# Kernel tuning notes

Hardware: AMD Instinct MI355X
Metric: run time of the kernel (lower is better)

The kernel has to match this reference:

```python
import jax, jax.numpy as jnp
import numpy as np

D_MODEL = 256
N_HEADS = 8
D_K = 16
LN_EPS = 1e-5


def setup_inputs() -> dict:
    key = jax.random.key(0)
    ks = jax.random.split(key, 10)
    B, S = 4, 2048
    inp = {
        "input_Q": jax.random.normal(ks[0], (B, S, D_MODEL), dtype=jnp.float32),
        "input_K": jax.random.normal(ks[1], (B, S, D_MODEL), dtype=jnp.float32),
        "input_V": jax.random.normal(ks[2], (B, S, D_MODEL), dtype=jnp.float32),
        "attn_mask": jax.random.randint(ks[3], (B, S, S), 0, 2) == 1,
        # learned params (torch Linear weight [out,in] stored here as [in,out])
        "Wq": jax.random.normal(ks[4], (D_MODEL, N_HEADS * D_K), dtype=jnp.float32) * (1.0 / np.sqrt(D_MODEL)),
        "Wk": jax.random.normal(ks[5], (D_MODEL, N_HEADS * D_K), dtype=jnp.float32) * (1.0 / np.sqrt(D_MODEL)),
        "Wv": jax.random.normal(ks[6], (D_MODEL, N_HEADS * D_K), dtype=jnp.float32) * (1.0 / np.sqrt(D_MODEL)),
        "Wfc": jax.random.normal(ks[7], (N_HEADS * D_K, D_MODEL), dtype=jnp.float32) * (1.0 / np.sqrt(N_HEADS * D_K)),
        "ln_gamma": jnp.ones((D_MODEL,), dtype=jnp.float32),
        "ln_beta": jnp.zeros((D_MODEL,), dtype=jnp.float32),
    }
    return inp


def reference(input_Q, input_K, input_V, attn_mask, Wq, Wk, Wv, Wfc, ln_gamma, ln_beta):
    B, S, _ = input_Q.shape
    # projections -> [B, H, S, d_k]
    Q = (input_Q @ Wq).reshape(B, S, N_HEADS, D_K).transpose(0, 2, 1, 3)
    K = (input_K @ Wk).reshape(B, S, N_HEADS, D_K).transpose(0, 2, 1, 3)
    V = (input_V @ Wv).reshape(B, S, N_HEADS, D_K).transpose(0, 2, 1, 3)
    # scores [B, H, S, S], masked softmax
    scores = jnp.einsum("bhqd,bhkd->bhqk", Q, K) / np.sqrt(D_K).astype(np.float32)
    scores = jnp.where(attn_mask[:, None, :, :], jnp.float32(-1e9), scores)
    attn = jax.nn.softmax(scores, axis=-1)
    context = jnp.einsum("bhqk,bhkd->bhqd", attn, V)
    context = context.transpose(0, 2, 1, 3).reshape(B, S, N_HEADS * D_K)
    out = context @ Wfc
    # LayerNorm (no residual in the original module)
    mu = jnp.mean(out, axis=-1, keepdims=True)
    var = jnp.var(out, axis=-1, keepdims=True)
    out = (out - mu) * jax.lax.rsqrt(var + LN_EPS) * ln_gamma + ln_beta
    return out
```

## Files before the change

### kernel.cpp

```cpp
#include <hip/hip_runtime.h>
#include <hip/hip_bf16.h>

#define S_LEN 2048
#define BATCH 4
#define NH 8
#define DK 16
#define DM 256
#define DP 128
#define L2E 1.4426950408889634f

typedef short bf16x8 __attribute__((ext_vector_type(8)));
typedef short short4v __attribute__((ext_vector_type(4)));
typedef float f32x16 __attribute__((ext_vector_type(16)));

__device__ __forceinline__ short f2bf(float x) {
    __hip_bfloat16 h = __float2bfloat16(x);
    return __builtin_bit_cast(short, h);
}

union Frag { bf16x8 v; short4v h2[2]; };

__global__ __launch_bounds__(256) void prep(
    const void* __restrict__ mraw, unsigned long long* __restrict__ ms64,
    const float* __restrict__ Wq, const float* __restrict__ Wk,
    const float* __restrict__ Wv, short* __restrict__ Wt,
    short* __restrict__ Vb)
{
    __shared__ int isBool;
    const int bi = blockIdx.x;
    const int t = threadIdx.x;

    if (bi < 512) {
        const int tid = bi * 256 + t;
        const int bh = tid >> 12;
        const int rem = tid & 4095;
        const int row = 16 + (rem >> 11) * 4;
        const int s = rem & 2047;
        Vb[((size_t)bh * 32 + row) * S_LEN + s] = (short)0x3F80;
    } else if (bi < 560) {
        const int tid = (bi - 512) * 256 + t;
        const int c  = tid & 127;
        const int hi = (tid >> 7) & 1;
        const int kb = (tid >> 8) & 15;
        const int m  = tid >> 12;
        const float* W = (m == 0) ? Wq : (m == 1) ? Wk : Wv;
        const float scale = (m == 0) ? 0.25f * L2E : 1.0f;
        const int k0 = kb * 16 + 4 * hi;
        union { bf16x8 v; short s[8]; } o;
        #pragma unroll
        for (int e = 0; e < 4; ++e) {
            o.s[e]     = f2bf(W[(size_t)(k0 + e) * DP + c] * scale);
            o.s[4 + e] = f2bf(W[(size_t)(k0 + 8 + e) * DP + c] * scale);
        }
        *(bf16x8*)(Wt + (size_t)tid * 8) = o.v;
    } else {
        const size_t kbase0 = (size_t)(bi - 560) * 4096;
        if (t == 0) isBool = 0;
        __syncthreads();
        {
            unsigned int u = ((const unsigned int*)mraw)[(kbase0 >> 2) + t * 4];
            if (u & 0xFFFFFF00u) isBool = 1;
        }
        __syncthreads();

        const int lane = t & 63;
        const size_t kbase = kbase0 + (size_t)(t >> 6) * 1024;
        int v[16];
        if (!isBool) {
            const int* p = (const int*)mraw + kbase + lane;
            #pragma unroll
            for (int g = 0; g < 16; ++g) v[g] = p[g * 64];
        } else {
            const unsigned char* p = (const unsigned char*)mraw + kbase + lane;
            #pragma unroll
            for (int g = 0; g < 16; ++g) v[g] = p[g * 64];
        }

        const size_t row = kbase >> 11;
        const int w0 = (int)(kbase & 2047) >> 6;

        unsigned long long myw = 0;
        #pragma unroll
        for (int g = 0; g < 16; ++g) {
            const unsigned long long W = __ballot(v[g] != 0);
            myw = (lane == g) ? W : myw;
        }
        if (lane < 16) ms64[row * 32 + w0 + lane] = myw;
    }
}

__global__ __launch_bounds__(256) void proj_mfma(
    const float* __restrict__ Xq, const float* __restrict__ Xk, const float* __restrict__ Xv,
    const short* __restrict__ Wt,
    short* __restrict__ Qt, short* __restrict__ Kb, short* __restrict__ Vb)
{
    __shared__ short xs_s[32 * 260];
    const int bi = blockIdx.x;
    const int t = threadIdx.x;
    const int inp = bi >> 8;
    const int s0 = (bi & 255) * 32;

    {
        const float* xbase = ((inp == 0) ? Xq : (inp == 1) ? Xk : Xv) + (size_t)s0 * 256;
        #pragma unroll
        for (int u = 0; u < 8; ++u) {
            const int idx = u * 1024 + t * 4;
            const int row = idx >> 8, col = idx & 255;
            float4 xv = *(const float4*)(xbase + idx);
            short4v o = { f2bf(xv.x), f2bf(xv.y), f2bf(xv.z), f2bf(xv.w) };
            *(short4v*)&xs_s[row * 260 + col] = o;
        }
    }

    const int wave = t >> 6, lane = t & 63;
    const int lq = lane & 31, hi = lane >> 5;
    const int c = wave * 32 + lq;

    const short* w2 = Wt + (((size_t)inp * 16 * 2 + hi) * 128 + c) * 8;
    Frag wf[16];
    #pragma unroll
    for (int kb = 0; kb < 16; ++kb)
        wf[kb].v = *(const bf16x8*)(w2 + (size_t)kb * 2048);
    asm volatile("" ::: "memory");
    __syncthreads();

    f32x16 acc;
    #pragma unroll
    for (int i = 0; i < 16; ++i) acc[i] = 0.f;

    #pragma unroll
    for (int kb = 0; kb < 16; ++kb) {
        Frag af;
        af.h2[0] = *(const short4v*)&xs_s[lq * 260 + kb*16 + 4*hi];
        af.h2[1] = *(const short4v*)&xs_s[lq * 260 + kb*16 + 8 + 4*hi];
        acc = __builtin_amdgcn_mfma_f32_32x32x16_bf16(af.v, wf[kb].v, acc, 0, 0, 0);
    }

    const int b = s0 >> 11, sl = s0 & (S_LEN - 1);
    const int h = c >> 4, d = c & 15;
    if (inp == 1) {
        #pragma unroll
        for (int r = 0; r < 16; ++r) {
            const int s = sl + (r & 3) + 8*(r >> 2) + 4*hi;
            Kb[(((size_t)(b * NH + h)) * S_LEN + s) * DK + d] = f2bf(acc[r]);
        }
    } else {
        short* base = (inp == 0)
            ? Qt + (((size_t)(b * NH + h)) * 16 + d) * S_LEN + sl
            : Vb + (((size_t)(b * NH + h)) * 32 + d) * S_LEN + sl;
        #pragma unroll
        for (int g = 0; g < 4; ++g) {
            short4v vv = { f2bf(acc[4*g]), f2bf(acc[4*g+1]), f2bf(acc[4*g+2]), f2bf(acc[4*g+3]) };
            *(short4v*)(base + 8*g + 4*hi) = vv;
        }
    }
}

__global__ __launch_bounds__(256, 8) void attn_mfma(
    const short* __restrict__ Qt, const short* __restrict__ Kb, const short* __restrict__ Vb,
    const unsigned long long* __restrict__ ms64, float* __restrict__ pacc, float* __restrict__ pl)
{
    __shared__ short kt_s[128 * 20];
    __shared__ short vt_s[32 * 132];

    const int bh = blockIdx.y;
    const int b = bh >> 3;
    const int z = blockIdx.z;
    const int t = threadIdx.x;
    const int wave = t >> 6, lane = t & 63;
    const int lq = lane & 31, hi = lane >> 5;
    const int qrow = blockIdx.x * 128 + wave * 32 + lq;

    Frag qf;
    {
        const short* qt = Qt + (size_t)bh * 16 * S_LEN + qrow;
        #pragma unroll
        for (int j = 0; j < 4; ++j) {
            qf.h2[0][j] = qt[(size_t)(4*hi + j) * S_LEN];
            qf.h2[1][j] = qt[(size_t)(8 + 4*hi + j) * S_LEN];
        }
    }

    f32x16 acc;
    #pragma unroll
    for (int i = 0; i < 16; ++i) acc[i] = 0.f;

    const short* kbase = Kb + (size_t)bh * S_LEN * DK;
    const short* vbase = Vb + (size_t)bh * 32 * S_LEN;
    const unsigned long long* mrow = ms64 + ((size_t)b * S_LEN + qrow) * 32;

    const int tiles = (S_LEN / 128) / gridDim.z;
    const int t0 = z * tiles, t1 = t0 + tiles;

    for (int tile = t0; tile < t1; ++tile) {
        const int k0 = tile * 128;

        {
            const uint4 kv = *(const uint4*)(kbase + (size_t)k0 * DK + t * 8);
            short* kdst = &kt_s[(t >> 1) * 20 + (t & 1) * 8];
            *(uint2*)(kdst)     = *(uint2*)&kv;
            *(uint2*)(kdst + 4) = *((uint2*)&kv + 1);

            const short* vsrc = vbase + (size_t)(t >> 3) * S_LEN + k0 + (t & 7) * 16;
            uint4 v0 = *(const uint4*)(vsrc);
            uint4 v1 = *(const uint4*)(vsrc + 8);
            short* vdst = &vt_s[(t >> 3) * 132 + (t & 7) * 16];
            *(uint2*)(vdst)      = *(uint2*)&v0;
            *(uint2*)(vdst + 4)  = *((uint2*)&v0 + 1);
            *(uint2*)(vdst + 8)  = *(uint2*)&v1;
            *(uint2*)(vdst + 12) = *((uint2*)&v1 + 1);
        }
        __syncthreads();

        const ulonglong2 mw = *(const ulonglong2*)(mrow + tile * 2);
        const unsigned long long W64a = mw.x, W64b = mw.y;

        #pragma unroll
        for (int kt = 0; kt < 4; ++kt) {
            const unsigned int W = (unsigned int)(((kt < 2) ? W64a : W64b)
                                                  >> (32*(kt & 1) + 4*hi));
            f32x16 ci;
            #pragma unroll
            for (int r = 0; r < 16; ++r) {
                const int bit = (r & 3) + 8*(r >> 2);
                ci[r] = __int_as_float(((int)(W << (31 - bit)) >> 31) & 0xC2C80000);
            }

            Frag kf;
            kf.h2[0] = *(const short4v*)&kt_s[(kt*32 + lq) * 20 + 4*hi];
            kf.h2[1] = *(const short4v*)&kt_s[(kt*32 + lq) * 20 + 8 + 4*hi];
            f32x16 p = __builtin_amdgcn_mfma_f32_32x32x16_bf16(kf.v, qf.v, ci, 0, 0, 0);

            #pragma unroll
            for (int r = 0; r < 16; ++r) p[r] = __builtin_amdgcn_exp2f(p[r]);

            #pragma unroll
            for (int j = 0; j < 2; ++j) {
                union { bf16x8 v; unsigned int u[4]; } pf;
                #pragma unroll
                for (int e = 0; e < 4; ++e) {
                    asm("v_cvt_pk_bf16_f32 %0, %1, %2"
                        : "=v"(pf.u[e]) : "v"(p[j*8 + 2*e]), "v"(p[j*8 + 2*e + 1]));
                }
                Frag vf;
                const int vo = lq * 132 + (kt*2 + j) * 16 + 4*hi;
                vf.h2[0] = *(const short4v*)&vt_s[vo];
                vf.h2[1] = *(const short4v*)&vt_s[vo + 8];
                acc = __builtin_amdgcn_mfma_f32_32x32x16_bf16(vf.v, pf.v, acc, 0, 0, 0);
            }
        }
        __syncthreads();
    }

    float* pb = pacc + (((size_t)z * (BATCH*NH) + bh) * S_LEN + qrow) * 16;
    float4 o1 = { acc[0], acc[1], acc[2], acc[3] };
    float4 o2 = { acc[4], acc[5], acc[6], acc[7] };
    *(float4*)(pb + 4*hi) = o1;
    *(float4*)(pb + 8 + 4*hi) = o2;
    if (hi == 0) pl[((size_t)z * (BATCH*NH) + bh) * S_LEN + qrow] = acc[8];
}

__global__ __launch_bounds__(256) void fc_ln(
    const float* __restrict__ pacc, const float* __restrict__ pl, int ns,
    const float* __restrict__ Wfc,
    const float* __restrict__ gamma, const float* __restrict__ beta,
    float* __restrict__ out)
{
    __shared__ float cs[8][DP];
    __shared__ float ys[8][256];
    __shared__ float red[16];
    const int t = threadIdx.x;
    const int row0 = blockIdx.x * 8;

    {
        const int idx = t * 4;
        const int r = idx >> 7, k = idx & 127;
        const int grow = row0 + r;
        const int b = grow >> 11, q = grow & (S_LEN - 1);
        const int h = k >> 4, d0 = k & 15;
        float4 s = {0.f, 0.f, 0.f, 0.f};
        float L = 0.f;
        for (int z = 0; z < ns; ++z) {
            const size_t o = ((size_t)z * (BATCH*NH) + b * NH + h) * S_LEN + q;
            const float4 a = *(const float4*)(pacc + o * 16 + d0);
            s.x += a.x; s.y += a.y; s.z += a.z; s.w += a.w;
            L += pl[o];
        }
        const float inv = 1.0f / L;
        float4 o4 = { s.x * inv, s.y * inv, s.z * inv, s.w * inv };
        *(float4*)&cs[r][k] = o4;
    }
    __syncthreads();

    float acc[8] = {0,0,0,0,0,0,0,0};
    for (int k = 0; k < DP; k += 4) {
        const float w0 = Wfc[(k+0)*DM + t];
        const float w1 = Wfc[(k+1)*DM + t];
        const float w2 = Wfc[(k+2)*DM + t];
        const float w3 = Wfc[(k+3)*DM + t];
        #pragma unroll
        for (int r = 0; r < 8; ++r) {
            float4 x = *(const float4*)&cs[r][k];
            acc[r] = fmaf(x.x, w0, fmaf(x.y, w1, fmaf(x.z, w2, fmaf(x.w, w3, acc[r]))));
        }
    }

    #pragma unroll
    for (int r = 0; r < 8; ++r) ys[r][t] = acc[r];
    __syncthreads();

    const int w = t >> 6, lj = t & 63;
    #pragma unroll
    for (int rr = 0; rr < 2; ++rr) {
        const int r = w * 2 + rr;
        float a0 = ys[r][lj], a1 = ys[r][lj+64], a2 = ys[r][lj+128], a3 = ys[r][lj+192];
        float s1 = a0 + a1 + a2 + a3;
        float s2 = a0*a0 + a1*a1 + a2*a2 + a3*a3;
        #pragma unroll
        for (int off = 32; off; off >>= 1) {
            s1 += __shfl_xor(s1, off);
            s2 += __shfl_xor(s2, off);
        }
        if (lj == 0) {
            float mu = s1 * (1.0f/256.0f);
            float var = s2 * (1.0f/256.0f) - mu*mu;
            red[r*2]     = mu;
            red[r*2 + 1] = rsqrtf(var + 1e-5f);
        }
    }
    __syncthreads();

    const float g = gamma[t], be = beta[t];
    #pragma unroll
    for (int r = 0; r < 8; ++r) {
        float y = (acc[r] - red[r*2]) * red[r*2 + 1];
        out[(size_t)(row0 + r) * DM + t] = fmaf(y, g, be);
    }
}

extern "C" void kernel_launch(void* const* d_in, const int* in_sizes, int n_in,
                              void* d_out, int out_size, void* d_ws, size_t ws_size,
                              hipStream_t stream)
{
    const float* Xq = (const float*)d_in[0];
    const float* Xk = (const float*)d_in[1];
    const float* Xv = (const float*)d_in[2];
    const void* mask_raw = d_in[3];
    const float* Wq  = (const float*)d_in[4];
    const float* Wk  = (const float*)d_in[5];
    const float* Wv  = (const float*)d_in[6];
    const float* Wfc = (const float*)d_in[7];
    const float* gamma = (const float*)d_in[8];
    const float* beta  = (const float*)d_in[9];
    float* out = (float*)d_out;

    const size_t headsz = (size_t)BATCH * NH * S_LEN * DK;
    const size_t maskelems = (size_t)BATCH * S_LEN * S_LEN;

    char* wsb = (char*)d_ws;
    short* Qt = (short*)wsb;
    short* Kb = Qt + headsz;
    short* Vb = Kb + headsz;
    unsigned long long* msk = (unsigned long long*)(Vb + 2 * headsz);
    short* Wt = (short*)(msk + maskelems / 64);
    float* pacc = (float*)(Wt + 3 * 128 * 256);
    size_t ns = 4;
    {
        const size_t fixed = (size_t)((char*)pacc - wsb);
        while (ns > 1 && fixed + ns * ((size_t)BATCH*NH*S_LEN*17*4) > ws_size)
            ns >>= 1;
    }
    float* pl = pacc + ns * (size_t)BATCH * NH * S_LEN * 16;

    prep<<<dim3(512 + 48 + (unsigned)(maskelems / 4096)), dim3(256), 0, stream>>>(
        mask_raw, msk, Wq, Wk, Wv, Wt, Vb);
    proj_mfma<<<dim3(768), dim3(256), 0, stream>>>(Xq, Xk, Xv, Wt, Qt, Kb, Vb);
    attn_mfma<<<dim3(S_LEN / 128, BATCH * NH, (unsigned)ns), dim3(256), 0, stream>>>(
        Qt, Kb, Vb, msk, pacc, pl);
    fc_ln<<<dim3(BATCH * S_LEN / 8), dim3(256), 0, stream>>>(pacc, pl, (int)ns, Wfc, gamma, beta, out);
}
```

Measured before the change: 72.85 us.

## Use MFMA for output projection and merge mask packing into projection kernel

Replaces the scalar fp32 FC+LayerNorm kernel with a bf16 MFMA version that handles 32 rows per block and does the LayerNorm reduction through shuffles and shared memory. Wfc is pre-converted to bf16 fragments in the prep kernel. Mask bit-packing moves out of prep and into the projection kernel's grid, so the mask packing and the Q/K/V projection run concurrently in one launch. This trades fp32 precision in the FC matmul for bf16 and changes the store pattern for the output.

```diff
diff --git a/kernel.cpp b/kernel.cpp
--- a/kernel.cpp
+++ b/kernel.cpp
@@ -21,12 +21,10 @@
 union Frag { bf16x8 v; short4v h2[2]; };
 
 __global__ __launch_bounds__(256) void prep(
-    const void* __restrict__ mraw, unsigned long long* __restrict__ ms64,
     const float* __restrict__ Wq, const float* __restrict__ Wk,
-    const float* __restrict__ Wv, short* __restrict__ Wt,
-    short* __restrict__ Vb)
+    const float* __restrict__ Wv, const float* __restrict__ Wfc,
+    short* __restrict__ Wt, short* __restrict__ Wfcb, short* __restrict__ Vb)
 {
-    __shared__ int isBool;
     const int bi = blockIdx.x;
     const int t = threadIdx.x;
 
@@ -54,7 +52,91 @@
         }
         *(bf16x8*)(Wt + (size_t)tid * 8) = o.v;
     } else {
-        const size_t kbase0 = (size_t)(bi - 560) * 4096;
+        const int tid = (bi - 560) * 256 + t;
+        const int c  = tid & 255;
+        const int hi = (tid >> 8) & 1;
+        const int kb = tid >> 9;
+        const int k0 = kb * 16 + 4 * hi;
+        union { bf16x8 v; short s[8]; } o;
+        #pragma unroll
+        for (int e = 0; e < 4; ++e) {
+            o.s[e]     = f2bf(Wfc[(size_t)(k0 + e) * DM + c]);
+            o.s[4 + e] = f2bf(Wfc[(size_t)(k0 + 8 + e) * DM + c]);
+        }
+        *(bf16x8*)(Wfcb + (size_t)tid * 8) = o.v;
+    }
+}
+
+__global__ __launch_bounds__(256) void main1(
+    const void* __restrict__ mraw, unsigned long long* __restrict__ ms64,
+    const float* __restrict__ Xq, const float* __restrict__ Xk, const float* __restrict__ Xv,
+    const short* __restrict__ Wt,
+    short* __restrict__ Qt, short* __restrict__ Kb, short* __restrict__ Vb)
+{
+    __shared__ short xs_s[32 * 260];
+    __shared__ int isBool;
+    const int bi = blockIdx.x;
+    const int t = threadIdx.x;
+
+    if (bi < 768) {
+        const int inp = bi >> 8;
+        const int s0 = (bi & 255) * 32;
+        {
+            const float* xbase = ((inp == 0) ? Xq : (inp == 1) ? Xk : Xv) + (size_t)s0 * 256;
+            #pragma unroll
+            for (int u = 0; u < 8; ++u) {
+                const int idx = u * 1024 + t * 4;
+                const int row = idx >> 8, col = idx & 255;
+                float4 xv = *(const float4*)(xbase + idx);
+                short4v o = { f2bf(xv.x), f2bf(xv.y), f2bf(xv.z), f2bf(xv.w) };
+                *(short4v*)&xs_s[row * 260 + col] = o;
+            }
+        }
+
+        const int wave = t >> 6, lane = t & 63;
+        const int lq = lane & 31, hi = lane >> 5;
+        const int c = wave * 32 + lq;
+
+        const short* w2 = Wt + (((size_t)inp * 16 * 2 + hi) * 128 + c) * 8;
+        Frag wf[16];
+        #pragma unroll
+        for (int kb = 0; kb < 16; ++kb)
+            wf[kb].v = *(const bf16x8*)(w2 + (size_t)kb * 2048);
+        asm volatile("" ::: "memory");
+        __syncthreads();
+
+        f32x16 acc;
+        #pragma unroll
+        for (int i = 0; i < 16; ++i) acc[i] = 0.f;
+
+        #pragma unroll
+        for (int kb = 0; kb < 16; ++kb) {
+            Frag af;
+            af.h2[0] = *(const short4v*)&xs_s[lq * 260 + kb*16 + 4*hi];
+            af.h2[1] = *(const short4v*)&xs_s[lq * 260 + kb*16 + 8 + 4*hi];
+            acc = __builtin_amdgcn_mfma_f32_32x32x16_bf16(af.v, wf[kb].v, acc, 0, 0, 0);
+        }
+
+        const int b = s0 >> 11, sl = s0 & (S_LEN - 1);
+        const int h = c >> 4, d = c & 15;
+        if (inp == 1) {
+            #pragma unroll
+            for (int r = 0; r < 16; ++r) {
+                const int s = sl + (r & 3) + 8*(r >> 2) + 4*hi;
+                Kb[(((size_t)(b * NH + h)) * S_LEN + s) * DK + d] = f2bf(acc[r]);
+            }
+        } else {
+            short* base = (inp == 0)
+                ? Qt + (((size_t)(b * NH + h)) * 16 + d) * S_LEN + sl
+                : Vb + (((size_t)(b * NH + h)) * 32 + d) * S_LEN + sl;
+            #pragma unroll
+            for (int g = 0; g < 4; ++g) {
+                short4v vv = { f2bf(acc[4*g]), f2bf(acc[4*g+1]), f2bf(acc[4*g+2]), f2bf(acc[4*g+3]) };
+                *(short4v*)(base + 8*g + 4*hi) = vv;
+            }
+        }
+    } else {
+        const size_t kbase0 = (size_t)(bi - 768) * 4096;
         if (t == 0) isBool = 0;
         __syncthreads();
         {
@@ -86,73 +168,6 @@
             myw = (lane == g) ? W : myw;
         }
         if (lane < 16) ms64[row * 32 + w0 + lane] = myw;
-    }
-}
-
-__global__ __launch_bounds__(256) void proj_mfma(
-    const float* __restrict__ Xq, const float* __restrict__ Xk, const float* __restrict__ Xv,
-    const short* __restrict__ Wt,
-    short* __restrict__ Qt, short* __restrict__ Kb, short* __restrict__ Vb)
-{
-    __shared__ short xs_s[32 * 260];
-    const int bi = blockIdx.x;
-    const int t = threadIdx.x;
-    const int inp = bi >> 8;
-    const int s0 = (bi & 255) * 32;
-
-    {
-        const float* xbase = ((inp == 0) ? Xq : (inp == 1) ? Xk : Xv) + (size_t)s0 * 256;
-        #pragma unroll
-        for (int u = 0; u < 8; ++u) {
-            const int idx = u * 1024 + t * 4;
-            const int row = idx >> 8, col = idx & 255;
-            float4 xv = *(const float4*)(xbase + idx);
-            short4v o = { f2bf(xv.x), f2bf(xv.y), f2bf(xv.z), f2bf(xv.w) };
-            *(short4v*)&xs_s[row * 260 + col] = o;
-        }
-    }
-
-    const int wave = t >> 6, lane = t & 63;
-    const int lq = lane & 31, hi = lane >> 5;
-    const int c = wave * 32 + lq;
-
-    const short* w2 = Wt + (((size_t)inp * 16 * 2 + hi) * 128 + c) * 8;
-    Frag wf[16];
-    #pragma unroll
-    for (int kb = 0; kb < 16; ++kb)
-        wf[kb].v = *(const bf16x8*)(w2 + (size_t)kb * 2048);
-    asm volatile("" ::: "memory");
-    __syncthreads();
-
-    f32x16 acc;
-    #pragma unroll
-    for (int i = 0; i < 16; ++i) acc[i] = 0.f;
-
-    #pragma unroll
-    for (int kb = 0; kb < 16; ++kb) {
-        Frag af;
-        af.h2[0] = *(const short4v*)&xs_s[lq * 260 + kb*16 + 4*hi];
-        af.h2[1] = *(const short4v*)&xs_s[lq * 260 + kb*16 + 8 + 4*hi];
-        acc = __builtin_amdgcn_mfma_f32_32x32x16_bf16(af.v, wf[kb].v, acc, 0, 0, 0);
-    }
-
-    const int b = s0 >> 11, sl = s0 & (S_LEN - 1);
-    const int h = c >> 4, d = c & 15;
-    if (inp == 1) {
-        #pragma unroll
-        for (int r = 0; r < 16; ++r) {
-            const int s = sl + (r & 3) + 8*(r >> 2) + 4*hi;
-            Kb[(((size_t)(b * NH + h)) * S_LEN + s) * DK + d] = f2bf(acc[r]);
-        }
-    } else {
-        short* base = (inp == 0)
-            ? Qt + (((size_t)(b * NH + h)) * 16 + d) * S_LEN + sl
-            : Vb + (((size_t)(b * NH + h)) * 32 + d) * S_LEN + sl;
-        #pragma unroll
-        for (int g = 0; g < 4; ++g) {
-            short4v vv = { f2bf(acc[4*g]), f2bf(acc[4*g+1]), f2bf(acc[4*g+2]), f2bf(acc[4*g+3]) };
-            *(short4v*)(base + 8*g + 4*hi) = vv;
-        }
     }
 }
 
@@ -194,7 +209,6 @@
 
     for (int tile = t0; tile < t1; ++tile) {
         const int k0 = tile * 128;
-
         {
             const uint4 kv = *(const uint4*)(kbase + (size_t)k0 * DK + t * 8);
             short* kdst = &kt_s[(t >> 1) * 20 + (t & 1) * 8];
@@ -260,81 +274,91 @@
     if (hi == 0) pl[((size_t)z * (BATCH*NH) + bh) * S_LEN + qrow] = acc[8];
 }
 
-__global__ __launch_bounds__(256) void fc_ln(
+__global__ __launch_bounds__(256) void fc_mfma(
     const float* __restrict__ pacc, const float* __restrict__ pl, int ns,
-    const float* __restrict__ Wfc,
+    const short* __restrict__ Wfcb,
     const float* __restrict__ gamma, const float* __restrict__ beta,
     float* __restrict__ out)
 {
-    __shared__ float cs[8][DP];
-    __shared__ float ys[8][256];
-    __shared__ float red[16];
+    __shared__ float red1[4][32], red2[4][32];
+    __shared__ float mu_s[32], rs_s[32];
+
     const int t = threadIdx.x;
-    const int row0 = blockIdx.x * 8;
-
-    {
-        const int idx = t * 4;
-        const int r = idx >> 7, k = idx & 127;
-        const int grow = row0 + r;
-        const int b = grow >> 11, q = grow & (S_LEN - 1);
-        const int h = k >> 4, d0 = k & 15;
-        float4 s = {0.f, 0.f, 0.f, 0.f};
-        float L = 0.f;
+    const int wave = t >> 6, lane = t & 63;
+    const int lq = lane & 31, hi = lane >> 5;
+    const int grow0 = blockIdx.x * 32;
+    const int b = grow0 >> 11;
+    const int q = (grow0 & (S_LEN - 1)) + lq;
+
+    Frag af[8];
+    #pragma unroll
+    for (int kb = 0; kb < 8; ++kb) {
+        float sx0=0,sx1=0,sx2=0,sx3=0, sy0=0,sy1=0,sy2=0,sy3=0, L=0;
         for (int z = 0; z < ns; ++z) {
-            const size_t o = ((size_t)z * (BATCH*NH) + b * NH + h) * S_LEN + q;
-            const float4 a = *(const float4*)(pacc + o * 16 + d0);
-            s.x += a.x; s.y += a.y; s.z += a.z; s.w += a.w;
+            const size_t o = ((size_t)z * (BATCH*NH) + b * NH + kb) * S_LEN + q;
+            const float4 a = *(const float4*)(pacc + o * 16 + 4*hi);
+            const float4 c2 = *(const float4*)(pacc + o * 16 + 8 + 4*hi);
+            sx0 += a.x; sx1 += a.y; sx2 += a.z; sx3 += a.w;
+            sy0 += c2.x; sy1 += c2.y; sy2 += c2.z; sy3 += c2.w;
             L += pl[o];
         }
         const float inv = 1.0f / L;
-        float4 o4 = { s.x * inv, s.y * inv, s.z * inv, s.w * inv };
-        *(float4*)&cs[r][k] = o4;
-    }
-    __syncthreads();
-
-    float acc[8] = {0,0,0,0,0,0,0,0};
-    for (int k = 0; k < DP; k += 4) {
-        const float w0 = Wfc[(k+0)*DM + t];
-        const float w1 = Wfc[(k+1)*DM + t];
-        const float w2 = Wfc[(k+2)*DM + t];
-        const float w3 = Wfc[(k+3)*DM + t];
-        #pragma unroll
-        for (int r = 0; r < 8; ++r) {
-            float4 x = *(const float4*)&cs[r][k];
-            acc[r] = fmaf(x.x, w0, fmaf(x.y, w1, fmaf(x.z, w2, fmaf(x.w, w3, acc[r]))));
-        }
-    }
-
-    #pragma unroll
-    for (int r = 0; r < 8; ++r) ys[r][t] = acc[r];
-    __syncthreads();
-
-    const int w = t >> 6, lj = t & 63;
-    #pragma unroll
-    for (int rr = 0; rr < 2; ++rr) {
-        const int r = w * 2 + rr;
-        float a0 = ys[r][lj], a1 = ys[r][lj+64], a2 = ys[r][lj+128], a3 = ys[r][lj+192];
-        float s1 = a0 + a1 + a2 + a3;
-        float s2 = a0*a0 + a1*a1 + a2*a2 + a3*a3;
-        #pragma unroll
-        for (int off = 32; off; off >>= 1) {
+        union { bf16x8 v; short s[8]; } o8;
+        o8.s[0] = f2bf(sx0*inv); o8.s[1] = f2bf(sx1*inv);
+        o8.s[2] = f2bf(sx2*inv); o8.s[3] = f2bf(sx3*inv);
+        o8.s[4] = f2bf(sy0*inv); o8.s[5] = f2bf(sy1*inv);
+        o8.s[6] = f2bf(sy2*inv); o8.s[7] = f2bf(sy3*inv);
+        af[kb].v = o8.v;
+    }
+
+    const int c0 = wave * 64 + lq, c1 = c0 + 32;
+    f32x16 acc0, acc1;
+    #pragma unroll
+    for (int i = 0; i < 16; ++i) { acc0[i] = 0.f; acc1[i] = 0.f; }
+
+    #pragma unroll
+    for (int kb = 0; kb < 8; ++kb) {
+        Frag b0, b1;
+        b0.v = *(const bf16x8*)(Wfcb + (size_t)(((kb*2 + hi) * 256) + c0) * 8);
+        b1.v = *(const bf16x8*)(Wfcb + (size_t)(((kb*2 + hi) * 256) + c1) * 8);
+        acc0 = __builtin_amdgcn_mfma_f32_32x32x16_bf16(af[kb].v, b0.v, acc0, 0, 0, 0);
+        acc1 = __builtin_amdgcn_mfma_f32_32x32x16_bf16(af[kb].v, b1.v, acc1, 0, 0, 0);
+    }
+
+    #pragma unroll
+    for (int r = 0; r < 16; ++r) {
+        float s1 = acc0[r] + acc1[r];
+        float s2 = acc0[r]*acc0[r] + acc1[r]*acc1[r];
+        #pragma unroll
+        for (int off = 16; off; off >>= 1) {
             s1 += __shfl_xor(s1, off);
             s2 += __shfl_xor(s2, off);
         }
-        if (lj == 0) {
-            float mu = s1 * (1.0f/256.0f);
-            float var = s2 * (1.0f/256.0f) - mu*mu;
-            red[r*2]     = mu;
-            red[r*2 + 1] = rsqrtf(var + 1e-5f);
+        if (lq == 0) {
+            const int row = (r & 3) + 8*(r >> 2) + 4*hi;
+            red1[wave][row] = s1;
+            red2[wave][row] = s2;
         }
     }
     __syncthreads();
-
-    const float g = gamma[t], be = beta[t];
-    #pragma unroll
-    for (int r = 0; r < 8; ++r) {
-        float y = (acc[r] - red[r*2]) * red[r*2 + 1];
-        out[(size_t)(row0 + r) * DM + t] = fmaf(y, g, be);
+    if (t < 32) {
+        const float s1 = red1[0][t] + red1[1][t] + red1[2][t] + red1[3][t];
+        const float s2 = red2[0][t] + red2[1][t] + red2[2][t] + red2[3][t];
+        const float mu = s1 * (1.0f/256.0f);
+        const float var = s2 * (1.0f/256.0f) - mu*mu;
+        mu_s[t] = mu;
+        rs_s[t] = rsqrtf(var + 1e-5f);
+    }
+    __syncthreads();
+
+    const float g0 = gamma[c0], be0 = beta[c0];
+    const float g1 = gamma[c1], be1 = beta[c1];
+    #pragma unroll
+    for (int r = 0; r < 16; ++r) {
+        const int row = (r & 3) + 8*(r >> 2) + 4*hi;
+        const float mu = mu_s[row], rs = rs_s[row];
+        out[(size_t)(grow0 + row) * DM + c0] = fmaf((acc0[r] - mu) * rs, g0, be0);
+        out[(size_t)(grow0 + row) * DM + c1] = fmaf((acc1[r] - mu) * rs, g1, be1);
     }
 }
 
@@ -363,7 +387,8 @@
     short* Vb = Kb + headsz;
     unsigned long long* msk = (unsigned long long*)(Vb + 2 * headsz);
     short* Wt = (short*)(msk + maskelems / 64);
-    float* pacc = (float*)(Wt + 3 * 128 * 256);
+    short* Wfcb = Wt + 3 * 128 * 256;
+    float* pacc = (float*)(Wfcb + 8 * 2 * 256 * 8);
     size_t ns = 4;
     {
         const size_t fixed = (size_t)((char*)pacc - wsb);
@@ -372,10 +397,11 @@
     }
     float* pl = pacc + ns * (size_t)BATCH * NH * S_LEN * 16;
 
-    prep<<<dim3(512 + 48 + (unsigned)(maskelems / 4096)), dim3(256), 0, stream>>>(
-        mask_raw, msk, Wq, Wk, Wv, Wt, Vb);
-    proj_mfma<<<dim3(768), dim3(256), 0, stream>>>(Xq, Xk, Xv, Wt, Qt, Kb, Vb);
+    prep<<<dim3(576), dim3(256), 0, stream>>>(Wq, Wk, Wv, Wfc, Wt, Wfcb, Vb);
+    main1<<<dim3(768 + (unsigned)(maskelems / 4096)), dim3(256), 0, stream>>>(
+        mask_raw, msk, Xq, Xk, Xv, Wt, Qt, Kb, Vb);
     attn_mfma<<<dim3(S_LEN / 128, BATCH * NH, (unsigned)ns), dim3(256), 0, stream>>>(
         Qt, Kb, Vb, msk, pacc, pl);
-    fc_ln<<<dim3(BATCH * S_LEN / 8), dim3(256), 0, stream>>>(pacc, pl, (int)ns, Wfc, gamma, beta, out);
-}
+    fc_mfma<<<dim3(BATCH * S_LEN / 32), dim3(256), 0, stream>>>(
+        pacc, pl, (int)ns, Wfcb, gamma, beta, out);
+}
```

New measurement: 80.78 us. +10.9%, slower.
